# Optimization experiments

Hardware: AMD Instinct MI355X
Metric: run time of the kernel (lower is better)

Reference implementation:

```python
import jax, jax.numpy as jnp
import numpy as np

B, T, C, H = 16, 2048, 1024, 64

def setup_inputs() -> dict:
    key = jax.random.key(0)
    kx, kq, kk, kv = jax.random.split(key, 4)
    x = jax.random.normal(kx, (B, T, C), dtype=jnp.float32)
    Wq = jax.random.normal(kq, (C, H), dtype=jnp.float32) * (C ** -0.5)
    Wk = jax.random.normal(kk, (C, H), dtype=jnp.float32) * (C ** -0.5)
    Wv = jax.random.normal(kv, (C, H), dtype=jnp.float32) * (C ** -0.5)
    return {"x": x, "Wq": Wq, "Wk": Wk, "Wv": Wv}

def reference(x, Wq, Wk, Wv):
    # single causal self-attention head; dropout p=0.0 (identity)
    Tlen = x.shape[1]
    q = jnp.einsum('btc,ch->bth', x, Wq)  # [B,T,H]
    k = jnp.einsum('btc,ch->bth', x, Wk)
    v = jnp.einsum('btc,ch->bth', x, Wv)
    scale = q.shape[-1] ** -0.5
    scores = jnp.einsum('bth,bsh->bts', q, k) * scale  # [B,T,T]
    causal = jnp.tril(jnp.ones((Tlen, Tlen), dtype=bool))
    scores = jnp.where(causal, scores, -jnp.inf)
    weights = jax.nn.softmax(scores, axis=-1)
    out = jnp.einsum('bts,bsh->bth', weights, v)  # [B,T,H]
    return out
```

## Files before the change

kernel.cpp:

```cpp
#include <hip/hip_runtime.h>


typedef float  floatx4 __attribute__((ext_vector_type(4)));
typedef __bf16 bf16x8  __attribute__((ext_vector_type(8)));
typedef short  short8v __attribute__((ext_vector_type(8)));
typedef unsigned short ushort4v __attribute__((ext_vector_type(4)));

constexpr int Bn = 16;
constexpr int Tn = 2048;
constexpr int Cn = 1024;
constexpr int Hn = 64;
constexpr int BT = Bn * Tn;

__device__ __forceinline__ unsigned short f2b(float f) {
  unsigned int u = __builtin_bit_cast(unsigned int, f);
  u += 0x7fffu + ((u >> 16) & 1u);
  return (unsigned short)(u >> 16);
}

__global__ __launch_bounds__(256) void pack_w(const float* __restrict__ Wq,
                                              const float* __restrict__ Wk,
                                              const float* __restrict__ Wv,
                                              unsigned short* __restrict__ Wp) {
  int gid = blockIdx.x * 256 + threadIdx.x;
  int mat = gid >> 16;
  int rem = gid & 65535;
  int k   = rem >> 6;
  int col = rem & 63;
  const float* W = (mat == 0) ? Wq : (mat == 1) ? Wk : Wv;
  float v = W[rem];
  int kb = k >> 3, j = k & 7, ct = (mat << 2) | (col >> 4), c = col & 15;
  size_t idx = ((((size_t)ct * 128) + kb) * 16 + c) * 8 + j;
  Wp[idx] = f2b(v);
}

__global__ __launch_bounds__(256) void proj_kernel(
    const float* __restrict__ x, const unsigned short* __restrict__ Wp,
    unsigned short* __restrict__ Q, unsigned short* __restrict__ K,
    unsigned short* __restrict__ Vt) {
  __shared__ alignas(16) unsigned short Al[64][72];
  __shared__ alignas(16) unsigned short Bl[12 * 1024];

  const int tid  = threadIdx.x;
  const int wave = tid >> 6;
  const int lane = tid & 63;
  const int quad = lane >> 4;
  const int l16  = lane & 15;
  const int wr   = wave >> 1;
  const int wc   = wave & 1;
  const int rbase = blockIdx.x * 64;

  floatx4 acc[2][6];
#pragma unroll
  for (int a = 0; a < 2; ++a)
#pragma unroll
    for (int b = 0; b < 6; ++b) acc[a][b] = (floatx4){0.f, 0.f, 0.f, 0.f};

  const int arow = tid >> 2;
  const int acol = (tid & 3) * 16;
  const float* xp = x + (size_t)(rbase + arow) * Cn + acol;

  for (int k0 = 0; k0 < Cn; k0 += 64) {
    floatx4 f0 = *reinterpret_cast<const floatx4*>(xp + k0);
    floatx4 f1 = *reinterpret_cast<const floatx4*>(xp + k0 + 4);
    floatx4 f2 = *reinterpret_cast<const floatx4*>(xp + k0 + 8);
    floatx4 f3 = *reinterpret_cast<const floatx4*>(xp + k0 + 12);

    if (k0) __syncthreads();

#pragma unroll
    for (int i = 0; i < 3; ++i) {
      const int ct = wave * 3 + i;
#pragma unroll
      for (int h = 0; h < 2; ++h) {
        const unsigned short* g =
            Wp + ((size_t)(ct * 128 + (k0 >> 3) + h * 4 + quad) * 16 + l16) * 8;
        __builtin_amdgcn_global_load_lds(
            (const __attribute__((address_space(1))) void*)g,
            (__attribute__((address_space(3))) void*)&Bl[ct * 1024 + h * 512],
            16, 0, 0);
      }
    }

    short8v p0, p1;
    p0[0] = (short)f2b(f0[0]); p0[1] = (short)f2b(f0[1]);
    p0[2] = (short)f2b(f0[2]); p0[3] = (short)f2b(f0[3]);
    p0[4] = (short)f2b(f1[0]); p0[5] = (short)f2b(f1[1]);
    p0[6] = (short)f2b(f1[2]); p0[7] = (short)f2b(f1[3]);
    p1[0] = (short)f2b(f2[0]); p1[1] = (short)f2b(f2[1]);
    p1[2] = (short)f2b(f2[2]); p1[3] = (short)f2b(f2[3]);
    p1[4] = (short)f2b(f3[0]); p1[5] = (short)f2b(f3[1]);
    p1[6] = (short)f2b(f3[2]); p1[7] = (short)f2b(f3[3]);
    *reinterpret_cast<short8v*>(&Al[arow][acol])     = p0;
    *reinterpret_cast<short8v*>(&Al[arow][acol + 8]) = p1;

    __syncthreads();

#pragma unroll
    for (int kk = 0; kk < 2; ++kk) {
      bf16x8 a0 = *reinterpret_cast<const bf16x8*>(
          &Al[wr * 32 + l16][kk * 32 + quad * 8]);
      bf16x8 a1 = *reinterpret_cast<const bf16x8*>(
          &Al[wr * 32 + 16 + l16][kk * 32 + quad * 8]);
#pragma unroll
      for (int c6 = 0; c6 < 6; ++c6) {
        const int ct = wc * 6 + c6;
        bf16x8 bfr = *reinterpret_cast<const bf16x8*>(
            &Bl[ct * 1024 + (kk * 4 + quad) * 128 + l16 * 8]);
        acc[0][c6] = __builtin_amdgcn_mfma_f32_16x16x32_bf16(a0, bfr, acc[0][c6], 0, 0, 0);
        acc[1][c6] = __builtin_amdgcn_mfma_f32_16x16x32_bf16(a1, bfr, acc[1][c6], 0, 0, 0);
      }
    }
  }

#pragma unroll
  for (int rt = 0; rt < 2; ++rt) {
#pragma unroll
    for (int c6 = 0; c6 < 6; ++c6) {
      const int cbase  = wc * 96 + c6 * 16;
      const int rowloc = wr * 32 + rt * 16 + quad * 4;
      if (cbase < 64) {
#pragma unroll
        for (int r = 0; r < 4; ++r)
          Q[(size_t)(rbase + rowloc + r) * Hn + cbase + l16] =
              f2b(acc[rt][c6][r] * 0.125f);
      } else if (cbase < 128) {
#pragma unroll
        for (int r = 0; r < 4; ++r)
          K[(size_t)(rbase + rowloc + r) * Hn + cbase - 64 + l16] =
              f2b(acc[rt][c6][r]);
      } else {
        const int b  = rbase >> 11;
        const int t0 = (rbase & 2047) + rowloc;
        const int h  = cbase - 128 + l16;
        ushort4v v;
#pragma unroll
        for (int r = 0; r < 4; ++r) v[r] = f2b(acc[rt][c6][r]);
        *reinterpret_cast<ushort4v*>(&Vt[((size_t)b * Hn + h) * Tn + t0]) = v;
      }
    }
  }
}

__global__ __launch_bounds__(256) void flash_kernel(
    const unsigned short* __restrict__ Q, const unsigned short* __restrict__ K,
    const unsigned short* __restrict__ Vt, float* __restrict__ out) {
  __shared__ alignas(16) unsigned short P[4][16][72];

  const int tid  = threadIdx.x;
  const int wave = tid >> 6;
  const int lane = tid & 63;
  const int quad = lane >> 4;
  const int l16  = lane & 15;

  const int b  = blockIdx.x & 15;
  const int qt = 31 - (blockIdx.x >> 4);
  const int qbase = qt * 64;
  const size_t bbase  = (size_t)b * Tn * Hn;
  const size_t vtbase = (size_t)b * Hn * Tn;

  bf16x8 qf[2];
#pragma unroll
  for (int i = 0; i < 2; ++i)
    qf[i] = *reinterpret_cast<const bf16x8*>(
        &Q[bbase + (size_t)(qbase + wave * 16 + l16) * Hn + i * 32 + quad * 8]);

  floatx4 O[4];
#pragma unroll
  for (int i = 0; i < 4; ++i) O[i] = (floatx4){0.f, 0.f, 0.f, 0.f};
  float m_r[4], l_r[4];
#pragma unroll
  for (int r = 0; r < 4; ++r) { m_r[r] = -INFINITY; l_r[r] = 0.f; }

  for (int kt = 0; kt <= qt; ++kt) {
    const int kvbase = kt * 64;

    floatx4 S[4];
#pragma unroll
    for (int ct = 0; ct < 4; ++ct) {
      floatx4 s = (floatx4){0.f, 0.f, 0.f, 0.f};
#pragma unroll
      for (int kk = 0; kk < 2; ++kk) {
        bf16x8 bfr = *reinterpret_cast<const bf16x8*>(
            &K[bbase + (size_t)(kvbase + ct * 16 + l16) * Hn + kk * 32 + quad * 8]);
        s = __builtin_amdgcn_mfma_f32_16x16x32_bf16(qf[kk], bfr, s, 0, 0, 0);
      }
      S[ct] = s;
    }

    bf16x8 vf[4][2];
#pragma unroll
    for (int ht = 0; ht < 4; ++ht)
#pragma unroll
      for (int kk = 0; kk < 2; ++kk)
        vf[ht][kk] = *reinterpret_cast<const bf16x8*>(
            &Vt[vtbase + (size_t)(ht * 16 + l16) * Tn + kvbase + kk * 32 + quad * 8]);

    if (kt == qt) {
#pragma unroll
      for (int ct = 0; ct < 4; ++ct)
#pragma unroll
        for (int r = 0; r < 4; ++r) {
          int trow = qbase + wave * 16 + quad * 4 + r;
          int scol = kvbase + ct * 16 + l16;
          if (scol > trow) S[ct][r] = -1e30f;
        }
    }

#pragma unroll
    for (int r = 0; r < 4; ++r) {
      float mx = fmaxf(fmaxf(S[0][r], S[1][r]), fmaxf(S[2][r], S[3][r]));
#pragma unroll
      for (int d = 1; d < 16; d <<= 1) mx = fmaxf(mx, __shfl_xor(mx, d));
      float mnew  = fmaxf(m_r[r], mx);
      float alpha = __expf(m_r[r] - mnew);
      float rs = 0.f;
#pragma unroll
      for (int ct = 0; ct < 4; ++ct) {
        float p = __expf(S[ct][r] - mnew);
        S[ct][r] = p;
        rs += p;
      }
#pragma unroll
      for (int d = 1; d < 16; d <<= 1) rs += __shfl_xor(rs, d);
      l_r[r] = l_r[r] * alpha + rs;
      m_r[r] = mnew;
#pragma unroll
      for (int ct = 0; ct < 4; ++ct) O[ct][r] *= alpha;
#pragma unroll
      for (int ct = 0; ct < 4; ++ct)
        P[wave][quad * 4 + r][ct * 16 + l16] = f2b(S[ct][r]);
    }

    bf16x8 pf0 = *reinterpret_cast<const bf16x8*>(&P[wave][l16][quad * 8]);
    bf16x8 pf1 = *reinterpret_cast<const bf16x8*>(&P[wave][l16][32 + quad * 8]);
#pragma unroll
    for (int ht = 0; ht < 4; ++ht) {
      O[ht] = __builtin_amdgcn_mfma_f32_16x16x32_bf16(pf0, vf[ht][0], O[ht], 0, 0, 0);
      O[ht] = __builtin_amdgcn_mfma_f32_16x16x32_bf16(pf1, vf[ht][1], O[ht], 0, 0, 0);
    }
  }

#pragma unroll
  for (int r = 0; r < 4; ++r) {
    float inv = 1.0f / l_r[r];
    int trow = qbase + wave * 16 + quad * 4 + r;
#pragma unroll
    for (int ht = 0; ht < 4; ++ht)
      out[bbase + (size_t)trow * Hn + ht * 16 + l16] = O[ht][r] * inv;
  }
}

extern "C" void kernel_launch(void* const* d_in, const int* in_sizes, int n_in,
                              void* d_out, int out_size, void* d_ws, size_t ws_size,
                              hipStream_t stream) {
  const float* x  = (const float*)d_in[0];
  const float* Wq = (const float*)d_in[1];
  const float* Wk = (const float*)d_in[2];
  const float* Wv = (const float*)d_in[3];
  float* out = (float*)d_out;

  char* ws = (char*)d_ws;
  unsigned short* Q  = (unsigned short*)(ws);
  unsigned short* Kb = (unsigned short*)(ws + ((size_t)4 << 20));
  unsigned short* Vt = (unsigned short*)(ws + ((size_t)8 << 20));
  unsigned short* Wp = (unsigned short*)(ws + ((size_t)12 << 20));

  pack_w<<<dim3(768), dim3(256), 0, stream>>>(Wq, Wk, Wv, Wp);
  proj_kernel<<<dim3(BT / 64), dim3(256), 0, stream>>>(x, Wp, Q, Kb, Vt);
  flash_kernel<<<dim3(512), dim3(256), 0, stream>>>(Q, Kb, Vt, out);
}
```

Measured before the change: 291.8 us.

## Split KV loop across waves per 16-row query block with LDS merge

Each block now handles 16 query rows instead of 64, and its four waves take interleaved KV tiles (split-K flash decoding within a block). The partial O, max and sum from each wave are combined through shared memory with a log-sum-exp rescale, and the result is written with vectorized stores. The grid grows from 512 to 2048 blocks, which improves load balance and occupancy on the causal triangle. In exchange, K/V tiles are reused by only 16 query rows instead of 64, so global/L2 traffic per FLOP rises, and the merge adds LDS work and a barrier.

```diff
diff --git a/kernel.cpp b/kernel.cpp
--- a/kernel.cpp
+++ b/kernel.cpp
@@ -146,6 +146,8 @@
     const unsigned short* __restrict__ Q, const unsigned short* __restrict__ K,
     const unsigned short* __restrict__ Vt, float* __restrict__ out) {
   __shared__ alignas(16) unsigned short P[4][16][72];
+  __shared__ alignas(16) float Om[4][16][68];
+  __shared__ float Ml[4][16][2];
 
   const int tid  = threadIdx.x;
   const int wave = tid >> 6;
@@ -153,9 +155,11 @@
   const int quad = lane >> 4;
   const int l16  = lane & 15;
 
-  const int b  = blockIdx.x & 15;
-  const int qt = 31 - (blockIdx.x >> 4);
-  const int qbase = qt * 64;
+  const int b   = blockIdx.x & 15;
+  const int p16 = 127 - (blockIdx.x >> 4);
+  const int qbase = p16 * 16;
+  const int n_tiles  = (p16 >> 2) + 1;
+  const int lastTile = p16 >> 2;
   const size_t bbase  = (size_t)b * Tn * Hn;
   const size_t vtbase = (size_t)b * Hn * Tn;
 
@@ -163,7 +167,7 @@
 #pragma unroll
   for (int i = 0; i < 2; ++i)
     qf[i] = *reinterpret_cast<const bf16x8*>(
-        &Q[bbase + (size_t)(qbase + wave * 16 + l16) * Hn + i * 32 + quad * 8]);
+        &Q[bbase + (size_t)(qbase + l16) * Hn + i * 32 + quad * 8]);
 
   floatx4 O[4];
 #pragma unroll
@@ -172,7 +176,7 @@
 #pragma unroll
   for (int r = 0; r < 4; ++r) { m_r[r] = -INFINITY; l_r[r] = 0.f; }
 
-  for (int kt = 0; kt <= qt; ++kt) {
+  for (int kt = wave; kt < n_tiles; kt += 4) {
     const int kvbase = kt * 64;
 
     floatx4 S[4];
@@ -196,12 +200,12 @@
         vf[ht][kk] = *reinterpret_cast<const bf16x8*>(
             &Vt[vtbase + (size_t)(ht * 16 + l16) * Tn + kvbase + kk * 32 + quad * 8]);
 
-    if (kt == qt) {
+    if (kt == lastTile) {
 #pragma unroll
       for (int ct = 0; ct < 4; ++ct)
 #pragma unroll
         for (int r = 0; r < 4; ++r) {
-          int trow = qbase + wave * 16 + quad * 4 + r;
+          int trow = qbase + quad * 4 + r;
           int scol = kvbase + ct * 16 + l16;
           if (scol > trow) S[ct][r] = -1e30f;
         }
@@ -242,12 +246,40 @@
   }
 
 #pragma unroll
-  for (int r = 0; r < 4; ++r) {
-    float inv = 1.0f / l_r[r];
-    int trow = qbase + wave * 16 + quad * 4 + r;
-#pragma unroll
-    for (int ht = 0; ht < 4; ++ht)
-      out[bbase + (size_t)trow * Hn + ht * 16 + l16] = O[ht][r] * inv;
+  for (int ht = 0; ht < 4; ++ht)
+#pragma unroll
+    for (int r = 0; r < 4; ++r)
+      Om[wave][quad * 4 + r][ht * 16 + l16] = O[ht][r];
+  if (l16 == 0) {
+#pragma unroll
+    for (int r = 0; r < 4; ++r) {
+      Ml[wave][quad * 4 + r][0] = m_r[r];
+      Ml[wave][quad * 4 + r][1] = l_r[r];
+    }
+  }
+  __syncthreads();
+
+  {
+    const int row = tid >> 4;
+    const int c4  = (tid & 15) * 4;
+    float m0 = Ml[0][row][0], m1 = Ml[1][row][0];
+    float m2 = Ml[2][row][0], m3 = Ml[3][row][0];
+    float M = fmaxf(fmaxf(m0, m1), fmaxf(m2, m3));
+    float e0 = __expf(m0 - M), e1 = __expf(m1 - M);
+    float e2 = __expf(m2 - M), e3 = __expf(m3 - M);
+    float L = Ml[0][row][1] * e0 + Ml[1][row][1] * e1 +
+              Ml[2][row][1] * e2 + Ml[3][row][1] * e3;
+    float invL = 1.0f / L;
+    floatx4 o0 = *reinterpret_cast<const floatx4*>(&Om[0][row][c4]);
+    floatx4 o1 = *reinterpret_cast<const floatx4*>(&Om[1][row][c4]);
+    floatx4 o2 = *reinterpret_cast<const floatx4*>(&Om[2][row][c4]);
+    floatx4 o3 = *reinterpret_cast<const floatx4*>(&Om[3][row][c4]);
+    floatx4 res;
+#pragma unroll
+    for (int j = 0; j < 4; ++j)
+      res[j] = (o0[j] * e0 + o1[j] * e1 + o2[j] * e2 + o3[j] * e3) * invL;
+    *reinterpret_cast<floatx4*>(
+        &out[bbase + (size_t)(qbase + row) * Hn + c4]) = res;
   }
 }
 
@@ -268,5 +300,5 @@
 
   pack_w<<<dim3(768), dim3(256), 0, stream>>>(Wq, Wk, Wv, Wp);
   proj_kernel<<<dim3(BT / 64), dim3(256), 0, stream>>>(x, Wp, Q, Kb, Vt);
-  flash_kernel<<<dim3(512), dim3(256), 0, stream>>>(Q, Kb, Vt, out);
-}
+  flash_kernel<<<dim3(16 * 128), dim3(256), 0, stream>>>(Q, Kb, Vt, out);
+}
```

New measurement: 270.8 us. -7.2%, faster.
